# Performance work log

Measured on AMD Instinct MI355X. Metric: run time of the kernel, lower is better.

## Reference

```python
import jax, jax.numpy as jnp
import numpy as np

SMOOTH = 1.0      # self.smooth
NUM_ITER = 10     # iter_
EPS = 1e-07
INF = 1e12        # stand-in for +inf in squared-distance init


def _maxpool(x, window):
    # torch max_pool3d(stride=1, padding=w//2): pad with -inf, window max
    pads = ((0, 0), (0, 0)) + tuple((w // 2, w // 2) for w in window)
    return jax.lax.reduce_window(x, -jnp.inf, jax.lax.max, (1, 1) + window, (1, 1, 1, 1, 1), pads)


def _soft_erode(x):  # x: [B,1,D,H,W]
    p1 = -_maxpool(-x, (3, 1, 1))
    p2 = -_maxpool(-x, (1, 3, 1))
    p3 = -_maxpool(-x, (1, 1, 3))
    return jnp.minimum(jnp.minimum(p1, p2), p3)


def _soft_open(x):
    return _maxpool(_soft_erode(x), (3, 3, 3))  # dilate(erode(x))


def _soft_skel(x, n_iter):
    skel = jax.nn.relu(x - _soft_open(x))
    for _ in range(n_iter):
        x = _soft_erode(x)
        delta = jax.nn.relu(x - _soft_open(x))
        skel = skel + jax.nn.relu(delta - skel * delta)
    return skel


def _edt_pass(d2, axis):
    # 1D squared-distance min-convolution: out[i] = min_j (i-j)^2 + d2[j]
    L = d2.shape[axis]
    d2m = jnp.moveaxis(d2, axis, -1)                 # [..., L]
    i = jnp.arange(L, dtype=d2.dtype)
    sq = (i[:, None] - i[None, :]) ** 2              # [L, L]
    out = jnp.min(d2m[..., None, :] + sq, axis=-1)   # [..., L]
    return jnp.moveaxis(out, -1, axis)


def _edt(mask):
    # exact Euclidean distance transform: distance of nonzero voxels to nearest zero voxel
    d2 = jnp.where(mask > 0, INF, 0.0).astype(jnp.float32)  # [B,D,H,W]
    for ax in (1, 2, 3):
        d2 = _edt_pass(d2, ax)
    return jnp.sqrt(d2)


def _get_weights(mask, skel):
    # mask, skel: [B,D,H,W] binary float
    dist = _edt(mask)
    dist = jnp.where(mask == 0, 0.0, dist)
    on_skel = skel == 1
    skel_r = jnp.where(on_skel, dist, 0.0)
    rmax = jnp.max(skel_r.reshape(skel_r.shape[0], -1), axis=1).reshape(-1, 1, 1, 1)
    valid = rmax > 0
    rmax_safe = jnp.where(valid, rmax, 1.0)
    dist_n = jnp.where(valid, dist / rmax_safe, dist)
    skel_rn = jnp.where(valid, skel_r / rmax_safe, skel_r)
    # dim == 3 branch: skel_1_R2_norm
    skel_1r2 = jnp.where(on_skel, (1.0 + EPS) / (skel_rn ** 2 + EPS), 0.0)
    return dist_n, skel_rn, skel_1r2


def _combine(A, B, C):
    # D = B*C, overwritten by A*C where (A != 0) & (B == 0)
    return jnp.where((A != 0) & (B == 0), A * C, B * C)


def reference(y_pred, y_true):
    # y_pred: [B,C,D,H,W] logits; y_true: [B,1,D,H,W] int labels
    fore = jnp.max(y_pred[:, 1:], axis=1, keepdims=True)
    logits = jnp.concatenate([y_pred[:, :1], fore], axis=1)   # [B,2,D,H,W]
    prob = jax.nn.softmax(logits, axis=1)
    yp = (prob[:, 1] > 0.5).astype(jnp.float32)               # [B,D,H,W]
    yt = (y_true > 0).astype(jnp.float32)[:, 0]               # [B,D,H,W]

    skel_p = _soft_skel(yp[:, None], NUM_ITER)[:, 0]
    skel_t = _soft_skel(yt[:, None], NUM_ITER)[:, 0]

    q_vl, q_slvl, q_sl = _get_weights(yt, skel_t)
    q_vp, q_spvp, q_sp = _get_weights(yp, skel_p)

    w_tprec = (jnp.sum(q_sp * q_vl) + SMOOTH) / (jnp.sum(_combine(q_spvp, q_slvl, q_sp)) + SMOOTH)
    w_tsens = (jnp.sum(q_sl * q_vp) + SMOOTH) / (jnp.sum(_combine(q_slvl, q_spvp, q_sl)) + SMOOTH)
    return 1.0 - 2.0 * (w_tprec * w_tsens) / (w_tprec + w_tsens)


def setup_inputs() -> dict:
    key = jax.random.key(0)
    k1, k2 = jax.random.split(key)
    y_pred = jax.random.normal(k1, (2, 2, 64, 96, 96), dtype=jnp.float32)
    y_true = jax.random.randint(k2, (2, 1, 64, 96, 96), 0, 2, dtype=jnp.int32)
    return {"y_pred": y_pred, "y_true": y_true}
```

## Files before the change

### kernel.cpp

```cpp
#include <hip/hip_runtime.h>

namespace {

constexpr int Bn = 2;
constexpr int Dn = 64;
constexpr int Hn = 96;
constexpr int Wn = 96;
constexpr int HW = Hn * Wn;
constexpr int S  = Dn * HW;
constexpr int NBS = Bn * S;
constexpr int NT  = 2 * NBS;
constexpr int WPR = Wn / 32;
constexpr int WPP = HW / 32;
constexpr int WPS = S / 32;
constexpr int NTW = NT / 32;
constexpr float INFD = 1e12f;
constexpr float EPSf = 1e-7f;
constexpr int TPB = 256;
constexpr int BLK_NBS = NBS / TPB;
constexpr int OPT = 8;
constexpr int BLK_EDT0 = NT / OPT / TPB;
constexpr int BLK_SUMS = NBS / 4 / TPB;

constexpr int skel_tot(int nup) {
  int t = 0;
  for (int k = 0; k <= nup; ++k)
    t += (2 * (nup - k) + 3) * (24 + 2 * (nup + 1 - k)) * 3;
  return t;
}

__global__ __launch_bounds__(TPB) void k_binarize(const float* __restrict__ logits,
                                                  const int* __restrict__ labels,
                                                  unsigned* __restrict__ Mb) {
  int idx = blockIdx.x * TPB + threadIdx.x;
  int b = idx / S;
  int s = idx - b * S;
  float l0 = logits[(b * 2 + 0) * S + s];
  float l1 = logits[(b * 2 + 1) * S + s];
  bool vp = l1 > l0;
  bool vt = labels[idx] > 0;
  unsigned long long mp = __ballot(vp);
  unsigned long long mt = __ballot(vt);
  int lane = threadIdx.x & 63;
  if (lane == 0) {
    Mb[idx >> 5]         = (unsigned)mp;
    Mb[(NBS + idx) >> 5] = (unsigned)mt;
  } else if (lane == 32) {
    Mb[idx >> 5]         = (unsigned)(mp >> 32);
    Mb[(NBS + idx) >> 5] = (unsigned)(mt >> 32);
  }
}

template <int NUP>
__global__ __launch_bounds__(TPB) void k_skel(const unsigned* __restrict__ x,
                                              unsigned* __restrict__ eout,
                                              unsigned* __restrict__ skel,
                                              int init) {
  constexpr int TOTW = skel_tot(NUP);
  constexpr int P0 = 2 * NUP + 3;
  constexpr int R0 = 24 + 2 * (NUP + 1);
  __shared__ unsigned shm[TOTW];
  __shared__ unsigned skbuf[72];
  int slab = blockIdx.x >> 8;
  int z = (blockIdx.x >> 2) & 63;
  int y0 = (blockIdx.x & 3) * 24;
  int tid = threadIdx.x;
  const unsigned* xs = x + slab * WPS;
  for (int t = tid; t < P0 * R0 * 3; t += TPB) {
    int p = t / (R0 * 3); int rem = t - p * (R0 * 3); int r = rem / 3; int wx = rem - r * 3;
    int zz = z - (NUP + 1) + p, yy = y0 - (NUP + 1) + r;
    shm[t] = (zz >= 0 && zz < Dn && yy >= 0 && yy < Hn)
               ? xs[zz * WPP + yy * WPR + wx] : 0xFFFFFFFFu;
  }
  for (int t = tid; t < 72; t += TPB) skbuf[t] = 0u;
  __syncthreads();
  int offPrev = 0;
  int offCur = P0 * R0 * 3;
  #pragma unroll
  for (int k = 1; k <= NUP; ++k) {
    const int Pk = 2 * (NUP - k) + 3, Rk = 24 + 2 * (NUP + 1 - k);
    const int Rp = Rk + 2;
    const int ps = Rp * 3;
    for (int t = tid; t < Pk * Rk * 3; t += TPB) {
      int p = t / (Rk * 3); int rem = t - p * (Rk * 3); int r = rem / 3; int wx = rem - r * 3;
      const unsigned* A = shm + offPrev;
      int ci = ((p + 1) * Rp + (r + 1)) * 3 + wx;
      unsigned v = A[ci];
      unsigned l = (v << 1) | (wx > 0 ? (A[ci - 1] >> 31) : 1u);
      unsigned rr = (v >> 1) | (wx < 2 ? (A[ci + 1] << 31) : 0x80000000u);
      shm[offCur + t] = v & l & rr & A[ci - 3] & A[ci + 3] & A[ci - ps] & A[ci + ps];
    }
    offPrev = offCur;
    offCur += Pk * Rk * 3;
    __syncthreads();
  }
  for (int t = tid; t < 72 * NUP; t += TPB) {
    int word = t % 72;
    int k = t / 72 + 1;
    int ro = word / 3, wx = word - ro * 3;
    int yy = y0 + ro;
    int offk = 0;
    for (int j = 0; j < k; ++j)
      offk += (2 * (NUP - j) + 3) * (24 + 2 * (NUP + 1 - j)) * 3;
    int Pk = 2 * (NUP - k) + 3, Rk = 24 + 2 * (NUP + 1 - k);
    int Pp = Pk + 2, Rp = Rk + 2;
    int offkm1 = offk - Pp * Rp * 3;
    const unsigned* A = shm + offk;
    int pc = (Pk - 1) / 2;
    int rb = ro + (NUP + 1 - k);
    unsigned acc = 0u;
    #pragma unroll
    for (int dz = -1; dz <= 1; ++dz) {
      if (z + dz < 0 || z + dz >= Dn) continue;
      #pragma unroll
      for (int dy = -1; dy <= 1; ++dy) {
        if (yy + dy < 0 || yy + dy >= Hn) continue;
        int ii = ((pc + dz) * Rk + (rb + dy)) * 3 + wx;
        unsigned c = A[ii];
        unsigned pw = (wx > 0) ? A[ii - 1] : 0u;
        unsigned nw = (wx < 2) ? A[ii + 1] : 0u;
        acc |= c | ((c << 1) | (pw >> 31)) | ((c >> 1) | (nw << 31));
      }
    }
    const unsigned* Ap = shm + offkm1;
    unsigned prevC = Ap[(((Pp - 1) / 2) * Rp + (ro + (NUP + 2 - k))) * 3 + wx];
    unsigned contrib = prevC & ~acc;
    if (contrib) atomicOr(&skbuf[word], contrib);
  }
  __syncthreads();
  for (int t = tid; t < 72; t += TPB) {
    int ro = t / 3, wx = t - ro * 3;
    unsigned ex = shm[TOTW - 234 + (26 + ro + 1) * 3 + wx];
    int gi = slab * WPS + z * WPP + (y0 + ro) * WPR + wx;
    eout[gi] = ex;
    unsigned sk = skbuf[t];
    skel[gi] = init ? sk : (skel[gi] | sk);
  }
}

__global__ __launch_bounds__(TPB) void k_edt0(const unsigned* __restrict__ Mb,
                                              float* __restrict__ out) {
  int gt = blockIdx.x * TPB + threadIdx.x;
  int c = gt % (4 * HW);
  int chunk = gt / (4 * HW);
  int slab = c / HW;
  int s2d = c - slab * HW;
  int i0 = chunk * OPT;
  const unsigned* mb = Mb + slab * WPS;
  float best[OPT];
  #pragma unroll
  for (int s = 0; s < OPT; ++s) best[s] = 3.4e38f;
  float db = (float)i0;
  #pragma unroll 4
  for (int j = 0; j < Dn; ++j) {
    int bi = j * HW + s2d;
    float f = ((mb[bi >> 5] >> (bi & 31)) & 1u) ? INFD : 0.0f;
    #pragma unroll
    for (int s = 0; s < OPT; ++s) {
      float d = db + (float)s;
      best[s] = fminf(best[s], fmaf(d, d, f));
    }
    db -= 1.0f;
  }
  float* o = out + slab * S + s2d;
  #pragma unroll
  for (int s = 0; s < OPT; ++s) o[(i0 + s) * HW] = best[s];
}

__global__ __launch_bounds__(TPB) void k_edt12(const float* __restrict__ D2,
                                               float* __restrict__ EF,
                                               const unsigned* __restrict__ skel,
                                               float* __restrict__ pmax) {
  __shared__ float Bh[24 * 97];
  __shared__ float ldsf[4];
  int slab = blockIdx.x >> 8;
  int z = (blockIdx.x >> 2) & 63;
  int y0 = (blockIdx.x & 3) * 24;
  int tid = threadIdx.x;
  int pb = slab * S + z * HW;
  for (int t = tid; t < 288; t += TPB) {
    int xx = t % 96;
    int c = t / 96;
    float best[OPT];
    #pragma unroll
    for (int s = 0; s < OPT; ++s) best[s] = 3.4e38f;
    float db = (float)(y0 + c * OPT);
    #pragma unroll 4
    for (int j = 0; j < Hn; ++j) {
      float f = D2[pb + j * 96 + xx];
      #pragma unroll
      for (int s = 0; s < OPT; ++s) {
        float d = db + (float)s;
        best[s] = fminf(best[s], fmaf(d, d, f));
      }
      db -= 1.0f;
    }
    #pragma unroll
    for (int s = 0; s < OPT; ++s) Bh[(c * OPT + s) * 97 + xx] = best[s];
  }
  __syncthreads();
  float m = 0.0f;
  for (int t = tid; t < 288; t += TPB) {
    int r = t / 12;
    int chunk = t - r * 12;
    int i0 = chunk * OPT;
    float best[OPT];
    #pragma unroll
    for (int s = 0; s < OPT; ++s) best[s] = 3.4e38f;
    float db = (float)i0;
    #pragma unroll 4
    for (int j = 0; j < Wn; ++j) {
      float f = Bh[r * 97 + j];
      #pragma unroll
      for (int s = 0; s < OPT; ++s) {
        float d = db + (float)s;
        best[s] = fminf(best[s], fmaf(d, d, f));
      }
      db -= 1.0f;
    }
    int gb = pb + (y0 + r) * 96 + i0;
    ((float4*)(EF + gb))[0] = make_float4(best[0], best[1], best[2], best[3]);
    ((float4*)(EF + gb))[1] = make_float4(best[4], best[5], best[6], best[7]);
    unsigned wv = skel[gb >> 5] >> (gb & 31);
    #pragma unroll
    for (int s = 0; s < OPT; ++s)
      if ((wv >> s) & 1u) m = fmaxf(m, best[s]);
  }
  #pragma unroll
  for (int o = 32; o > 0; o >>= 1) m = fmaxf(m, __shfl_xor(m, o, 64));
  if ((tid & 63) == 0) ldsf[tid >> 6] = m;
  __syncthreads();
  if (tid == 0)
    pmax[blockIdx.x] = fmaxf(fmaxf(ldsf[0], ldsf[1]), fmaxf(ldsf[2], ldsf[3]));
}

__global__ __launch_bounds__(TPB) void k_sums(const float* __restrict__ d2,
                                              const unsigned* __restrict__ skel,
                                              const float* __restrict__ pmax,
                                              double* __restrict__ ps) {
  __shared__ float lmax[4];
  __shared__ double ldsd[4][4];
  int tid = threadIdx.x;
  {
    int wave = tid >> 6, lane = tid & 63;
    const float* pw = pmax + wave * 256;
    float v = fmaxf(fmaxf(pw[lane], pw[lane + 64]),
                    fmaxf(pw[lane + 128], pw[lane + 192]));
    #pragma unroll
    for (int o = 32; o > 0; o >>= 1) v = fmaxf(v, __shfl_xor(v, o, 64));
    if (lane == 0) lmax[wave] = v;
  }
  __syncthreads();
  int q = blockIdx.x * TPB + tid;
  int idx0 = q * 4;
  int b = idx0 / S;
  float rmax_p = sqrtf(lmax[b]);
  float rmax_t = sqrtf(lmax[2 + b]);
  float4 dp4 = ((const float4*)d2)[q];
  float4 dt4 = ((const float4*)(d2 + NBS))[q];
  unsigned spw = (skel[idx0 >> 5] >> (idx0 & 31)) & 0xFu;
  unsigned stw = (skel[(NBS + idx0) >> 5] >> (idx0 & 31)) & 0xFu;
  const float* dp = &dp4.x;
  const float* dt = &dt4.x;
  double acc[4] = {0.0, 0.0, 0.0, 0.0};
  #pragma unroll
  for (int s = 0; s < 4; ++s) {
    float dist_p = sqrtf(dp[s]);
    float dist_t = sqrtf(dt[s]);
    bool sp = (spw >> s) & 1u;
    bool st = (stw >> s) & 1u;
    float q_vp = (rmax_p > 0.0f) ? dist_p / rmax_p : dist_p;
    float q_vl = (rmax_t > 0.0f) ? dist_t / rmax_t : dist_t;
    float q_spvp = sp ? q_vp : 0.0f;
    float q_slvl = st ? q_vl : 0.0f;
    float q_sp = sp ? (1.0f + EPSf) / (q_spvp * q_spvp + EPSf) : 0.0f;
    float q_sl = st ? (1.0f + EPSf) / (q_slvl * q_slvl + EPSf) : 0.0f;
    acc[0] += (double)(q_sp * q_vl);
    acc[1] += (double)(((q_spvp != 0.0f) && (q_slvl == 0.0f)) ? q_spvp * q_sp
                                                              : q_slvl * q_sp);
    acc[2] += (double)(q_sl * q_vp);
    acc[3] += (double)(((q_slvl != 0.0f) && (q_spvp == 0.0f)) ? q_slvl * q_sl
                                                              : q_spvp * q_sl);
  }
  #pragma unroll
  for (int k = 0; k < 4; ++k)
    #pragma unroll
    for (int o = 32; o > 0; o >>= 1)
      acc[k] += __shfl_xor(acc[k], o, 64);
  if ((tid & 63) == 0) {
    #pragma unroll
    for (int k = 0; k < 4; ++k) ldsd[tid >> 6][k] = acc[k];
  }
  __syncthreads();
  if (tid == 0) {
    #pragma unroll
    for (int k = 0; k < 4; ++k)
      ps[blockIdx.x * 4 + k] = ldsd[0][k] + ldsd[1][k] + ldsd[2][k] + ldsd[3][k];
  }
}

__global__ __launch_bounds__(TPB) void k_final(const double* __restrict__ ps,
                                               float* __restrict__ out) {
  __shared__ double ldsd[4][4];
  int tid = threadIdx.x;
  double s[4] = {0.0, 0.0, 0.0, 0.0};
  for (int i = tid; i < BLK_SUMS; i += TPB) {
    s[0] += ps[i * 4 + 0];
    s[1] += ps[i * 4 + 1];
    s[2] += ps[i * 4 + 2];
    s[3] += ps[i * 4 + 3];
  }
  #pragma unroll
  for (int k = 0; k < 4; ++k)
    #pragma unroll
    for (int o = 32; o > 0; o >>= 1)
      s[k] += __shfl_xor(s[k], o, 64);
  if ((tid & 63) == 0) {
    #pragma unroll
    for (int k = 0; k < 4; ++k) ldsd[tid >> 6][k] = s[k];
  }
  __syncthreads();
  if (tid == 0) {
    double tot[4];
    #pragma unroll
    for (int k = 0; k < 4; ++k)
      tot[k] = ldsd[0][k] + ldsd[1][k] + ldsd[2][k] + ldsd[3][k];
    double wp = (tot[0] + 1.0) / (tot[1] + 1.0);
    double ws = (tot[2] + 1.0) / (tot[3] + 1.0);
    out[0] = (float)(1.0 - 2.0 * (wp * ws) / (wp + ws));
  }
}

}

extern "C" void kernel_launch(void* const* d_in, const int* in_sizes, int n_in,
                              void* d_out, int out_size, void* d_ws, size_t ws_size,
                              hipStream_t stream) {
  (void)in_sizes; (void)n_in; (void)out_size; (void)ws_size;
  const float* logits = (const float*)d_in[0];
  const int* labels   = (const int*)d_in[1];
  float* out = (float*)d_out;

  float* D2 = (float*)d_ws;
  float* EF = D2 + NT;
  unsigned* MB    = (unsigned*)(EF + NT);
  unsigned* XB    = MB + NTW;
  unsigned* EB    = XB + NTW;
  unsigned* SKELB = EB + NTW;
  float* PMAX  = (float*)(SKELB + NTW);
  double* PS   = (double*)(PMAX + 1024);

  dim3 blk(TPB);

  k_binarize<<<BLK_NBS, blk, 0, stream>>>(logits, labels, MB);

  k_skel<4><<<1024, blk, 0, stream>>>(MB, XB, SKELB, 1);
  k_skel<4><<<1024, blk, 0, stream>>>(XB, EB, SKELB, 0);
  k_skel<3><<<1024, blk, 0, stream>>>(EB, XB, SKELB, 0);

  k_edt0<<<BLK_EDT0, blk, 0, stream>>>(MB, D2);
  k_edt12<<<1024, blk, 0, stream>>>(D2, EF, SKELB, PMAX);

  k_sums<<<BLK_SUMS, blk, 0, stream>>>(EF, SKELB, PMAX, PS);
  k_final<<<1, blk, 0, stream>>>(PS, out);
}
```

Baseline: 141.2 us.

## Fuse binarize with depth EDT, single-pass 11-iteration skeleton, retile EDT12

Binarization and the first EDT pass now run in one kernel: per-column bits are kept in shared memory, so the depth pass no longer re-reads the bit mask from global memory. The three chained skeleton kernels become one kernel. It loads a 12-voxel halo and ping-pongs erosions in two LDS buffers, dilating a separable OR, and keeps the skeleton bits in registers, which removes the intermediate erosion buffers and two launches. The H/W EDT kernel moves to 192 threads computing 12 outputs each. The cost is more redundant halo work per block, larger LDS use, and many barriers in the skeleton loop.

```diff
diff --git a/kernel.cpp b/kernel.cpp
--- a/kernel.cpp
+++ b/kernel.cpp
@@ -16,203 +16,184 @@
 constexpr int NTW = NT / 32;
 constexpr float INFD = 1e12f;
 constexpr float EPSf = 1e-7f;
-constexpr int TPB = 256;
-constexpr int BLK_NBS = NBS / TPB;
-constexpr int OPT = 8;
-constexpr int BLK_EDT0 = NT / OPT / TPB;
-constexpr int BLK_SUMS = NBS / 4 / TPB;
-
-constexpr int skel_tot(int nup) {
-  int t = 0;
-  for (int k = 0; k <= nup; ++k)
-    t += (2 * (nup - k) + 3) * (24 + 2 * (nup + 1 - k)) * 3;
-  return t;
-}
-
-__global__ __launch_bounds__(TPB) void k_binarize(const float* __restrict__ logits,
+constexpr int BLK_SUMS = NBS / 4 / 256;
+
+__global__ __launch_bounds__(256) void k_bin_edt0(const float* __restrict__ logits,
                                                   const int* __restrict__ labels,
-                                                  unsigned* __restrict__ Mb) {
-  int idx = blockIdx.x * TPB + threadIdx.x;
-  int b = idx / S;
-  int s = idx - b * S;
-  float l0 = logits[(b * 2 + 0) * S + s];
-  float l1 = logits[(b * 2 + 1) * S + s];
-  bool vp = l1 > l0;
-  bool vt = labels[idx] > 0;
-  unsigned long long mp = __ballot(vp);
-  unsigned long long mt = __ballot(vt);
-  int lane = threadIdx.x & 63;
-  if (lane == 0) {
-    Mb[idx >> 5]         = (unsigned)mp;
-    Mb[(NBS + idx) >> 5] = (unsigned)mt;
-  } else if (lane == 32) {
-    Mb[idx >> 5]         = (unsigned)(mp >> 32);
-    Mb[(NBS + idx) >> 5] = (unsigned)(mt >> 32);
-  }
-}
-
-template <int NUP>
-__global__ __launch_bounds__(TPB) void k_skel(const unsigned* __restrict__ x,
-                                              unsigned* __restrict__ eout,
-                                              unsigned* __restrict__ skel,
-                                              int init) {
-  constexpr int TOTW = skel_tot(NUP);
-  constexpr int P0 = 2 * NUP + 3;
-  constexpr int R0 = 24 + 2 * (NUP + 1);
-  __shared__ unsigned shm[TOTW];
-  __shared__ unsigned skbuf[72];
+                                                  unsigned* __restrict__ Mb,
+                                                  float* __restrict__ D2) {
+  __shared__ unsigned bits[64];
+  int slab = blockIdx.x / 288;
+  int cg = blockIdx.x - slab * 288;
+  int c0 = cg * 32;
+  int tid = threadIdx.x;
+  int lane = tid & 63;
+  for (int t = tid; t < 2048; t += 256) {
+    int zz = t >> 5;
+    int col = t & 31;
+    int s = zz * HW + c0 + col;
+    bool v;
+    if (slab < 2) {
+      float l0 = logits[(slab * 2 + 0) * S + s];
+      float l1 = logits[(slab * 2 + 1) * S + s];
+      v = l1 > l0;
+    } else {
+      v = labels[(slab - 2) * S + s] > 0;
+    }
+    unsigned long long m = __ballot(v);
+    if (lane == 0) {
+      unsigned w = (unsigned)m;
+      bits[zz] = w;
+      Mb[slab * WPS + zz * WPP + cg] = w;
+    } else if (lane == 32) {
+      unsigned w = (unsigned)(m >> 32);
+      bits[zz] = w;
+      Mb[slab * WPS + zz * WPP + cg] = w;
+    }
+  }
+  __syncthreads();
+  int col = tid & 31;
+  int chunk = tid >> 5;
+  int i0 = chunk * 8;
+  float best[8];
+  #pragma unroll
+  for (int s = 0; s < 8; ++s) best[s] = 3.4e38f;
+  float db = (float)i0;
+  #pragma unroll 4
+  for (int j = 0; j < Dn; ++j) {
+    float f = ((bits[j] >> col) & 1u) ? INFD : 0.0f;
+    #pragma unroll
+    for (int s = 0; s < 8; ++s) {
+      float d = db + (float)s;
+      best[s] = fminf(best[s], fmaf(d, d, f));
+    }
+    db -= 1.0f;
+  }
+  float* o = D2 + slab * S + c0 + col;
+  #pragma unroll
+  for (int s = 0; s < 8; ++s) o[(i0 + s) * HW] = best[s];
+}
+
+__global__ __launch_bounds__(256) void k_skel11(const unsigned* __restrict__ x,
+                                                unsigned* __restrict__ skel) {
+  __shared__ unsigned bufA[3600];
+  __shared__ unsigned bufB[3174];
+  __shared__ unsigned Sbuf[72];
   int slab = blockIdx.x >> 8;
   int z = (blockIdx.x >> 2) & 63;
   int y0 = (blockIdx.x & 3) * 24;
   int tid = threadIdx.x;
   const unsigned* xs = x + slab * WPS;
-  for (int t = tid; t < P0 * R0 * 3; t += TPB) {
-    int p = t / (R0 * 3); int rem = t - p * (R0 * 3); int r = rem / 3; int wx = rem - r * 3;
-    int zz = z - (NUP + 1) + p, yy = y0 - (NUP + 1) + r;
-    shm[t] = (zz >= 0 && zz < Dn && yy >= 0 && yy < Hn)
-               ? xs[zz * WPP + yy * WPR + wx] : 0xFFFFFFFFu;
-  }
-  for (int t = tid; t < 72; t += TPB) skbuf[t] = 0u;
-  __syncthreads();
-  int offPrev = 0;
-  int offCur = P0 * R0 * 3;
-  #pragma unroll
-  for (int k = 1; k <= NUP; ++k) {
-    const int Pk = 2 * (NUP - k) + 3, Rk = 24 + 2 * (NUP + 1 - k);
-    const int Rp = Rk + 2;
-    const int ps = Rp * 3;
-    for (int t = tid; t < Pk * Rk * 3; t += TPB) {
-      int p = t / (Rk * 3); int rem = t - p * (Rk * 3); int r = rem / 3; int wx = rem - r * 3;
-      const unsigned* A = shm + offPrev;
-      int ci = ((p + 1) * Rp + (r + 1)) * 3 + wx;
-      unsigned v = A[ci];
-      unsigned l = (v << 1) | (wx > 0 ? (A[ci - 1] >> 31) : 1u);
-      unsigned rr = (v >> 1) | (wx < 2 ? (A[ci + 1] << 31) : 0x80000000u);
-      shm[offCur + t] = v & l & rr & A[ci - 3] & A[ci + 3] & A[ci - ps] & A[ci + ps];
-    }
-    offPrev = offCur;
-    offCur += Pk * Rk * 3;
+  for (int t = tid; t < 25 * 48 * 3; t += 256) {
+    int p = t / 144;
+    int rem = t - p * 144;
+    int r = rem / 3;
+    int wx = rem - r * 3;
+    int zz = z - 12 + p, yy = y0 - 12 + r;
+    bufA[t] = (zz >= 0 && zz < Dn && yy >= 0 && yy < Hn)
+                ? xs[zz * WPP + yy * WPR + wx] : 0xFFFFFFFFu;
+  }
+  __syncthreads();
+  unsigned skreg = 0u;
+  int ro = tid / 3, wxo = tid - ro * 3;
+  int yyo = y0 + ro;
+  #pragma unroll
+  for (int k = 1; k <= 11; ++k) {
+    unsigned* src = (k & 1) ? bufA : bufB;
+    unsigned* dst = (k & 1) ? bufB : bufA;
+    const int Rs = 50 - 2 * k;
+    const int Pd = 25 - 2 * k, Rd = 48 - 2 * k;
+    const int ps = Rs * 3;
+    for (int t = tid; t < Pd * Rd * 3; t += 256) {
+      int p = t / (Rd * 3);
+      int rem = t - p * (Rd * 3);
+      int r = rem / 3;
+      int wx = rem - r * 3;
+      int ci = ((p + 1) * Rs + (r + 1)) * 3 + wx;
+      unsigned v = src[ci];
+      unsigned l = (v << 1) | (wx > 0 ? (src[ci - 1] >> 31) : 1u);
+      unsigned rr = (v >> 1) | (wx < 2 ? (src[ci + 1] << 31) : 0x80000000u);
+      dst[t] = v & l & rr & src[ci - 3] & src[ci + 3] & src[ci - ps] & src[ci + ps];
+    }
     __syncthreads();
-  }
-  for (int t = tid; t < 72 * NUP; t += TPB) {
-    int word = t % 72;
-    int k = t / 72 + 1;
-    int ro = word / 3, wx = word - ro * 3;
-    int yy = y0 + ro;
-    int offk = 0;
-    for (int j = 0; j < k; ++j)
-      offk += (2 * (NUP - j) + 3) * (24 + 2 * (NUP + 1 - j)) * 3;
-    int Pk = 2 * (NUP - k) + 3, Rk = 24 + 2 * (NUP + 1 - k);
-    int Pp = Pk + 2, Rp = Rk + 2;
-    int offkm1 = offk - Pp * Rp * 3;
-    const unsigned* A = shm + offk;
-    int pc = (Pk - 1) / 2;
-    int rb = ro + (NUP + 1 - k);
-    unsigned acc = 0u;
-    #pragma unroll
-    for (int dz = -1; dz <= 1; ++dz) {
-      if (z + dz < 0 || z + dz >= Dn) continue;
+    if (tid < 72) {
+      const int pc = 12 - k;
+      const int rb = ro + 12 - k;
+      unsigned s = 0u;
       #pragma unroll
-      for (int dy = -1; dy <= 1; ++dy) {
-        if (yy + dy < 0 || yy + dy >= Hn) continue;
-        int ii = ((pc + dz) * Rk + (rb + dy)) * 3 + wx;
-        unsigned c = A[ii];
-        unsigned pw = (wx > 0) ? A[ii - 1] : 0u;
-        unsigned nw = (wx < 2) ? A[ii + 1] : 0u;
-        acc |= c | ((c << 1) | (pw >> 31)) | ((c >> 1) | (nw << 31));
+      for (int dz = -1; dz <= 1; ++dz) {
+        if (z + dz < 0 || z + dz >= Dn) continue;
+        #pragma unroll
+        for (int dy = -1; dy <= 1; ++dy) {
+          if (yyo + dy < 0 || yyo + dy >= Hn) continue;
+          s |= dst[((pc + dz) * Rd + (rb + dy)) * 3 + wxo];
+        }
       }
-    }
-    const unsigned* Ap = shm + offkm1;
-    unsigned prevC = Ap[(((Pp - 1) / 2) * Rp + (ro + (NUP + 2 - k))) * 3 + wx];
-    unsigned contrib = prevC & ~acc;
-    if (contrib) atomicOr(&skbuf[word], contrib);
-  }
-  __syncthreads();
-  for (int t = tid; t < 72; t += TPB) {
-    int ro = t / 3, wx = t - ro * 3;
-    unsigned ex = shm[TOTW - 234 + (26 + ro + 1) * 3 + wx];
-    int gi = slab * WPS + z * WPP + (y0 + ro) * WPR + wx;
-    eout[gi] = ex;
-    unsigned sk = skbuf[t];
-    skel[gi] = init ? sk : (skel[gi] | sk);
-  }
-}
-
-__global__ __launch_bounds__(TPB) void k_edt0(const unsigned* __restrict__ Mb,
-                                              float* __restrict__ out) {
-  int gt = blockIdx.x * TPB + threadIdx.x;
-  int c = gt % (4 * HW);
-  int chunk = gt / (4 * HW);
-  int slab = c / HW;
-  int s2d = c - slab * HW;
-  int i0 = chunk * OPT;
-  const unsigned* mb = Mb + slab * WPS;
-  float best[OPT];
-  #pragma unroll
-  for (int s = 0; s < OPT; ++s) best[s] = 3.4e38f;
-  float db = (float)i0;
-  #pragma unroll 4
-  for (int j = 0; j < Dn; ++j) {
-    int bi = j * HW + s2d;
-    float f = ((mb[bi >> 5] >> (bi & 31)) & 1u) ? INFD : 0.0f;
-    #pragma unroll
-    for (int s = 0; s < OPT; ++s) {
-      float d = db + (float)s;
-      best[s] = fminf(best[s], fmaf(d, d, f));
-    }
-    db -= 1.0f;
-  }
-  float* o = out + slab * S + s2d;
-  #pragma unroll
-  for (int s = 0; s < OPT; ++s) o[(i0 + s) * HW] = best[s];
-}
-
-__global__ __launch_bounds__(TPB) void k_edt12(const float* __restrict__ D2,
+      Sbuf[tid] = s;
+    }
+    __syncthreads();
+    if (tid < 72) {
+      unsigned s = Sbuf[tid];
+      unsigned pw = (wxo > 0) ? Sbuf[tid - 1] : 0u;
+      unsigned nw = (wxo < 2) ? Sbuf[tid + 1] : 0u;
+      unsigned acc = s | ((s << 1) | (pw >> 31)) | ((s >> 1) | (nw << 31));
+      unsigned prevC = src[((13 - k) * Rs + (ro + 13 - k)) * 3 + wxo];
+      skreg |= prevC & ~acc;
+    }
+    __syncthreads();
+  }
+  if (tid < 72) {
+    int gi = slab * WPS + z * WPP + yyo * WPR + wxo;
+    skel[gi] = skreg;
+  }
+}
+
+__global__ __launch_bounds__(192) void k_edt12(const float* __restrict__ D2,
                                                float* __restrict__ EF,
                                                const unsigned* __restrict__ skel,
                                                float* __restrict__ pmax) {
   __shared__ float Bh[24 * 97];
-  __shared__ float ldsf[4];
+  __shared__ float ldsf[3];
   int slab = blockIdx.x >> 8;
-  int z = (blockIdx.x >> 2) & 63;
+  int zz = (blockIdx.x >> 2) & 63;
   int y0 = (blockIdx.x & 3) * 24;
   int tid = threadIdx.x;
-  int pb = slab * S + z * HW;
-  for (int t = tid; t < 288; t += TPB) {
-    int xx = t % 96;
-    int c = t / 96;
-    float best[OPT];
-    #pragma unroll
-    for (int s = 0; s < OPT; ++s) best[s] = 3.4e38f;
-    float db = (float)(y0 + c * OPT);
+  int pb = slab * S + zz * HW;
+  {
+    int xx = tid % 96;
+    int c = tid / 96;
+    float best[12];
+    #pragma unroll
+    for (int s = 0; s < 12; ++s) best[s] = 3.4e38f;
+    float db = (float)(y0 + c * 12);
     #pragma unroll 4
     for (int j = 0; j < Hn; ++j) {
       float f = D2[pb + j * 96 + xx];
       #pragma unroll
-      for (int s = 0; s < OPT; ++s) {
+      for (int s = 0; s < 12; ++s) {
         float d = db + (float)s;
         best[s] = fminf(best[s], fmaf(d, d, f));
       }
       db -= 1.0f;
     }
     #pragma unroll
-    for (int s = 0; s < OPT; ++s) Bh[(c * OPT + s) * 97 + xx] = best[s];
+    for (int s = 0; s < 12; ++s) Bh[(c * 12 + s) * 97 + xx] = best[s];
   }
   __syncthreads();
   float m = 0.0f;
-  for (int t = tid; t < 288; t += TPB) {
-    int r = t / 12;
-    int chunk = t - r * 12;
-    int i0 = chunk * OPT;
-    float best[OPT];
-    #pragma unroll
-    for (int s = 0; s < OPT; ++s) best[s] = 3.4e38f;
+  {
+    int r = tid >> 3;
+    int chunk = tid & 7;
+    int i0 = chunk * 12;
+    float best[12];
+    #pragma unroll
+    for (int s = 0; s < 12; ++s) best[s] = 3.4e38f;
     float db = (float)i0;
     #pragma unroll 4
     for (int j = 0; j < Wn; ++j) {
       float f = Bh[r * 97 + j];
       #pragma unroll
-      for (int s = 0; s < OPT; ++s) {
+      for (int s = 0; s < 12; ++s) {
         float d = db + (float)s;
         best[s] = fminf(best[s], fmaf(d, d, f));
       }
@@ -221,20 +202,25 @@
     int gb = pb + (y0 + r) * 96 + i0;
     ((float4*)(EF + gb))[0] = make_float4(best[0], best[1], best[2], best[3]);
     ((float4*)(EF + gb))[1] = make_float4(best[4], best[5], best[6], best[7]);
-    unsigned wv = skel[gb >> 5] >> (gb & 31);
-    #pragma unroll
-    for (int s = 0; s < OPT; ++s)
-      if ((wv >> s) & 1u) m = fmaxf(m, best[s]);
+    ((float4*)(EF + gb))[2] = make_float4(best[8], best[9], best[10], best[11]);
+    int sh = gb & 31;
+    unsigned w0 = skel[gb >> 5];
+    unsigned w1 = (sh + 11 > 31) ? skel[(gb >> 5) + 1] : 0u;
+    unsigned long long wv = ((unsigned long long)w1 << 32) | (unsigned long long)w0;
+    unsigned bitsv = (unsigned)(wv >> sh);
+    #pragma unroll
+    for (int s = 0; s < 12; ++s)
+      if ((bitsv >> s) & 1u) m = fmaxf(m, best[s]);
   }
   #pragma unroll
   for (int o = 32; o > 0; o >>= 1) m = fmaxf(m, __shfl_xor(m, o, 64));
   if ((tid & 63) == 0) ldsf[tid >> 6] = m;
   __syncthreads();
   if (tid == 0)
-    pmax[blockIdx.x] = fmaxf(fmaxf(ldsf[0], ldsf[1]), fmaxf(ldsf[2], ldsf[3]));
-}
-
-__global__ __launch_bounds__(TPB) void k_sums(const float* __restrict__ d2,
+    pmax[blockIdx.x] = fmaxf(fmaxf(ldsf[0], ldsf[1]), ldsf[2]);
+}
+
+__global__ __launch_bounds__(256) void k_sums(const float* __restrict__ d2,
                                               const unsigned* __restrict__ skel,
                                               const float* __restrict__ pmax,
                                               double* __restrict__ ps) {
@@ -251,7 +237,7 @@
     if (lane == 0) lmax[wave] = v;
   }
   __syncthreads();
-  int q = blockIdx.x * TPB + tid;
+  int q = blockIdx.x * 256 + tid;
   int idx0 = q * 4;
   int b = idx0 / S;
   float rmax_p = sqrtf(lmax[b]);
@@ -299,12 +285,12 @@
   }
 }
 
-__global__ __launch_bounds__(TPB) void k_final(const double* __restrict__ ps,
+__global__ __launch_bounds__(256) void k_final(const double* __restrict__ ps,
                                                float* __restrict__ out) {
   __shared__ double ldsd[4][4];
   int tid = threadIdx.x;
   double s[4] = {0.0, 0.0, 0.0, 0.0};
-  for (int i = tid; i < BLK_SUMS; i += TPB) {
+  for (int i = tid; i < BLK_SUMS; i += 256) {
     s[0] += ps[i * 4 + 0];
     s[1] += ps[i * 4 + 1];
     s[2] += ps[i * 4 + 2];
@@ -344,23 +330,13 @@
   float* D2 = (float*)d_ws;
   float* EF = D2 + NT;
   unsigned* MB    = (unsigned*)(EF + NT);
-  unsigned* XB    = MB + NTW;
-  unsigned* EB    = XB + NTW;
-  unsigned* SKELB = EB + NTW;
+  unsigned* SKELB = MB + NTW;
   float* PMAX  = (float*)(SKELB + NTW);
   double* PS   = (double*)(PMAX + 1024);
 
-  dim3 blk(TPB);
-
-  k_binarize<<<BLK_NBS, blk, 0, stream>>>(logits, labels, MB);
-
-  k_skel<4><<<1024, blk, 0, stream>>>(MB, XB, SKELB, 1);
-  k_skel<4><<<1024, blk, 0, stream>>>(XB, EB, SKELB, 0);
-  k_skel<3><<<1024, blk, 0, stream>>>(EB, XB, SKELB, 0);
-
-  k_edt0<<<BLK_EDT0, blk, 0, stream>>>(MB, D2);
-  k_edt12<<<1024, blk, 0, stream>>>(D2, EF, SKELB, PMAX);
-
-  k_sums<<<BLK_SUMS, blk, 0, stream>>>(EF, SKELB, PMAX, PS);
-  k_final<<<1, blk, 0, stream>>>(PS, out);
-}
+  k_bin_edt0<<<1152, 256, 0, stream>>>(logits, labels, MB, D2);
+  k_skel11<<<1024, 256, 0, stream>>>(MB, SKELB);
+  k_edt12<<<1024, 192, 0, stream>>>(D2, EF, SKELB, PMAX);
+  k_sums<<<1152, 256, 0, stream>>>(EF, SKELB, PMAX, PS);
+  k_final<<<1, 256, 0, stream>>>(PS, out);
+}
```

New measurement: 140.8 us. About the same (-0.3%).
